# Kernel optimization log

Measured on AMD Instinct MI355X. Metric: run time of the kernel, lower is better.

The kernel has to match this reference:

```python
import jax, jax.numpy as jnp
import numpy as np

NUM_SPHERICAL = 7
NUM_RADIAL = 6
CUTOFF = 5.0
ENVELOPE_EXPONENT = 5
ENVELOPE_CUTOFF = 5.0  # hardcoded in the torch module: poly_envelop(cutoff=5.0, ...)
E = 1_000_000   # num edges
T = 4_000_000   # num triplets (angles)


def _jn_np(l, x):
    """Spherical Bessel j_l(x) in numpy via upward recurrence (x > 0)."""
    j0 = np.sin(x) / x
    if l == 0:
        return j0
    j1 = np.sin(x) / x ** 2 - np.cos(x) / x
    for i in range(2, l + 1):
        j0, j1 = j1, (2 * i - 1) / x * j1 - j0
    return j1


def _jn_zeros(n, k):
    """First k positive zeros of j_l for l=0..n-1 (zeros interlace)."""
    zeros = np.zeros((n, k))
    prev = np.arange(1, k + n) * np.pi  # zeros of j_0
    zeros[0] = prev[:k]
    for l in range(1, n):
        cur = []
        for i in range(len(prev) - 1):
            a, b = prev[i], prev[i + 1]
            fa = _jn_np(l, a)
            for _ in range(80):  # bisection
                m = 0.5 * (a + b)
                fm = _jn_np(l, m)
                if np.sign(fm) == np.sign(fa):
                    a, fa = m, fm
                else:
                    b = m
            cur.append(0.5 * (a + b))
        prev = np.array(cur)
        zeros[l] = prev[:k]
    return zeros


# constants derived from (num_spherical, num_radial) at build time
Z = _jn_zeros(NUM_SPHERICAL, NUM_RADIAL)  # [S, R] Bessel zeros z_{l,n}
NORM = np.array([[np.sqrt(2.0) / abs(_jn_np(l + 1, Z[l, n])) for n in range(NUM_RADIAL)]
                 for l in range(NUM_SPHERICAL)])  # [S, R]
Y_NORM = np.array([np.sqrt((2 * l + 1) / (4.0 * np.pi)) for l in range(NUM_SPHERICAL)])  # m=0 SH norms


def _spherical_jn(l, a):
    """j_l(a) in jax via upward recurrence."""
    j0 = jnp.sin(a) / a
    if l == 0:
        return j0
    j1 = jnp.sin(a) / a ** 2 - jnp.cos(a) / a
    for i in range(2, l + 1):
        j0, j1 = j1, (2 * i - 1) / a * j1 - j0
    return j1


def _envelope(d):
    """DimeNet polynomial envelope, p = exponent + 1, on u = d / cutoff."""
    p = ENVELOPE_EXPONENT + 1
    a = -(p + 1) * (p + 2) / 2.0
    b = float(p * (p + 2))
    c = -p * (p + 1) / 2.0
    u = d / ENVELOPE_CUTOFF
    env = 1.0 / u + a * u ** (p - 1) + b * u ** p + c * u ** (p + 1)
    return jnp.where(u < 1.0, env, 0.0)


def setup_inputs() -> dict:
    key = jax.random.key(0)
    k1, k2, k3 = jax.random.split(key, 3)
    d = jax.random.uniform(k1, (E,), jnp.float32, 0.5, CUTOFF)           # edge distances
    Angles = jax.random.uniform(k2, (T,), jnp.float32, 0.0, float(np.pi))  # triplet angles
    edge_index_1 = jax.random.randint(k3, (T,), 0, E, dtype=jnp.int64 if jax.config.jax_enable_x64 else jnp.int32)
    return {"d": d, "Angles": Angles, "edge_index_1": edge_index_1}


def reference(d, Angles, edge_index_1):
    S, R = NUM_SPHERICAL, NUM_RADIAL
    zeros = jnp.asarray(Z, d.dtype)     # [S, R]
    norm = jnp.asarray(NORM, d.dtype)   # [S, R]
    x = d / CUTOFF                      # [E]
    # radial basis: norm_{l,n} * j_l(z_{l,n} * x)  -> [E, S, R]
    rbf = jnp.stack([norm[l] * _spherical_jn(l, zeros[l][None, :] * x[:, None])
                     for l in range(S)], axis=1)
    rbf_env = (_envelope(d)[:, None, None] * rbf).reshape(d.shape[0], S * R)  # [E, S*R]
    rbf_env = rbf_env[edge_index_1]  # gather triplets -> [T, S*R]
    # angular basis: Y_l^0(theta) = sqrt((2l+1)/4pi) * P_l(cos theta)
    c = jnp.cos(Angles)
    P = [jnp.ones_like(c), c]
    for l in range(2, S):
        P.append(((2 * l - 1) * c * P[l - 1] - (l - 1) * P[l - 2]) / l)
    y_norm = jnp.asarray(Y_NORM, c.dtype)
    cbf = jnp.stack([y_norm[l] * P[l] for l in range(S)], axis=1)  # [T, S]
    cbf = jnp.repeat(cbf, R, axis=1)  # repeat_interleave -> [T, S*R]
    return rbf_env * cbf
```

## Files before the change

kernel.cpp:

```cpp
#include <hip/hip_runtime.h>
#include <hip/hip_bf16.h>
#include <hip/hip_fp16.h>
#include <math.h>

#define NSPH 7
#define NRAD 6
#define NJ 42
#define BLK 256

typedef float v2 __attribute__((ext_vector_type(2)));
typedef float v4 __attribute__((ext_vector_type(4)));

struct KC {
  float zf[NJ];
  float izf[NJ];
  float nyf[NJ];
  float sc5[7];
  float sc6[7];
};

__global__ void __launch_bounds__(BLK, 4) k_fused(const float* __restrict__ d,
                                                  const float* __restrict__ ang,
                                                  const int* __restrict__ idx,
                                                  float* __restrict__ out,
                                                  int T, KC C) {
  __shared__ __half sv[BLK * NJ];
  const int tid = threadIdx.x;
  const int t0 = blockIdx.x * BLK;
  const int t = t0 + tid;

  if (t < T) {
    const int e = __builtin_nontemporal_load(idx + t);
    const float an = __builtin_nontemporal_load(ang + t);
    const float dv = d[e];

    const float x = dv * 0.2f;
    const float invx = __builtin_amdgcn_rcpf(x);
    const float x2 = x * x;
    const float x5 = x2 * x2 * x;
    float env = invx + x5 * fmaf(x, fmaf(x, -21.0f, 48.0f), -28.0f);
    if (x >= 1.0f) env = 0.0f;

    const float cth = __cosf(an);
    float mP[NSPH];
    {
      float p0 = 1.f, p1 = cth;
      mP[0] = env; mP[1] = env * cth;
      const float rl[5] = {1.f/2.f, 1.f/3.f, 1.f/4.f, 1.f/5.f, 1.f/6.f};
      #pragma unroll
      for (int l = 2; l < NSPH; ++l) {
        float pn = (fmaf((float)(2*l-1) * cth, p1, -(float)(l-1) * p0)) * rl[l-2];
        mP[l] = env * pn;
        p0 = p1; p1 = pn;
      }
    }

    __half* row = sv + tid * NJ;

    #pragma unroll
    for (int l = 0; l < 5; ++l) {
      #pragma unroll
      for (int p = 0; p < 3; ++p) {
        const int i = l * NRAD + 2 * p;
        v2 z    = {C.zf[i],  C.zf[i+1]};
        v2 iz   = {C.izf[i], C.izf[i+1]};
        v2 ny   = {C.nyf[i], C.nyf[i+1]};
        v2 a    = z * x;
        v2 s;  s.x = __sinf(a.x);  s.y = __sinf(a.y);
        v2 inva = iz * invx;
        v2 j0   = s * inva;
        v2 jl;
        if (l == 0) {
          jl = j0;
        } else {
          v2 c;  c.x = __cosf(a.x);  c.y = __cosf(a.y);
          v2 j1 = (j0 - c) * inva;
          #pragma unroll
          for (int m = 2; m <= l; ++m) {
            v2 jn_ = ((float)(2*m-1) * inva) * j1 - j0;
            j0 = j1; j1 = jn_;
          }
          jl = j1;
        }
        v2 jv = (ny * jl) * mP[l];
        *(__half2*)(row + i) = __float22half2_rn((float2){jv.x, jv.y});
      }
    }

    #pragma unroll
    for (int l = 5; l < NSPH; ++l) {
      const float* sc = (l == 5) ? C.sc5 : C.sc6;
      #pragma unroll
      for (int p = 0; p < 3; ++p) {
        const int i = l * NRAD + 2 * p;
        v2 z    = {C.zf[i],  C.zf[i+1]};
        v2 iz   = {C.izf[i], C.izf[i+1]};
        v2 ny   = {C.nyf[i], C.nyf[i+1]};
        v2 a    = z * x;
        v2 s;  s.x = __sinf(a.x);  s.y = __sinf(a.y);
        v2 c;  c.x = __cosf(a.x);  c.y = __cosf(a.y);
        v2 inva = iz * invx;
        v2 j0   = s * inva;
        v2 j1   = (j0 - c) * inva;
        #pragma unroll
        for (int m = 2; m <= l; ++m) {
          v2 jn_ = ((float)(2*m-1) * inva) * j1 - j0;
          j0 = j1; j1 = jn_;
        }
        v2 u  = a * a;
        v2 pp = u * sc[6] + sc[5];
        pp = u * pp + sc[4];
        pp = u * pp + sc[3];
        pp = u * pp + sc[2];
        pp = u * pp + sc[1];
        pp = u * pp + sc[0];
        v2 u2 = u * u;
        v2 al = (l == 5) ? (u2 * a) : (u2 * u);
        v2 jser = al * pp;
        v2 jl;
        jl.x = (a.x < 4.0f) ? jser.x : j1.x;
        jl.y = (a.y < 4.0f) ? jser.y : j1.y;
        v2 jv = (ny * jl) * mP[l];
        *(__half2*)(row + i) = __float22half2_rn((float2){jv.x, jv.y});
      }
    }
  }
  __syncthreads();

  const int nwords = (((T - t0) < BLK ? (T - t0) : BLK)) * NJ;
  const int nv4 = nwords >> 2;
  float* ob = out + (size_t)t0 * NJ;
  #pragma unroll
  for (int k = 0; k < 11; ++k) {
    int w4 = k * BLK + tid;
    if (w4 < nv4) {
      uint2 hh = *(const uint2*)((const unsigned char*)sv + 8u * (unsigned)w4);
      float2 r0 = __half22float2(*(__half2*)&hh.x);
      float2 r1 = __half22float2(*(__half2*)&hh.y);
      *(v4*)(ob + 4 * w4) = (v4){r0.x, r0.y, r1.x, r1.y};
    }
  }
  {
    int rem = nwords - (nv4 << 2);
    if (tid < rem) {
      int wd = (nv4 << 2) + tid;
      ob[wd] = __half2float(sv[wd]);
    }
  }
}

static double jn_host(int l, double x) {
  double j0 = sin(x) / x;
  if (l == 0) return j0;
  double j1 = sin(x) / (x * x) - cos(x) / x;
  for (int i = 2; i <= l; ++i) {
    double jn_ = (2 * i - 1) / x * j1 - j0;
    j0 = j1; j1 = jn_;
  }
  return j1;
}

extern "C" void kernel_launch(void* const* d_in, const int* in_sizes, int n_in,
                              void* d_out, int out_size, void* d_ws, size_t ws_size,
                              hipStream_t stream) {
  const float* d   = (const float*)d_in[0];
  const float* ang = (const float*)d_in[1];
  const int*   idx = (const int*)d_in[2];
  float* out = (float*)d_out;
  const int T = in_sizes[1];

  KC C;
  {
    const double PI = 3.14159265358979323846;
    double zeros[NSPH][NRAD];
    double prev[NSPH + NRAD - 1];
    int np_ = NSPH + NRAD - 1;
    for (int i = 0; i < np_; ++i) prev[i] = (i + 1) * PI;
    for (int j = 0; j < NRAD; ++j) zeros[0][j] = prev[j];
    for (int l = 1; l < NSPH; ++l) {
      int nc = np_ - 1;
      double cur[NSPH + NRAD - 1];
      for (int i = 0; i < nc; ++i) {
        double a = prev[i], b = prev[i + 1];
        double fa = jn_host(l, a);
        for (int it = 0; it < 80; ++it) {
          double m = 0.5 * (a + b);
          double fm = jn_host(l, m);
          if ((fm > 0.0) == (fa > 0.0)) { a = m; fa = fm; } else { b = m; }
        }
        cur[i] = 0.5 * (a + b);
      }
      for (int i = 0; i < nc; ++i) prev[i] = cur[i];
      np_ = nc;
      for (int j = 0; j < NRAD; ++j) zeros[l][j] = prev[j];
    }
    for (int l = 0; l < NSPH; ++l) {
      double yn = sqrt((2.0 * l + 1.0) / (4.0 * PI));
      for (int n = 0; n < NRAD; ++n) {
        int i = l * NRAD + n;
        double z = zeros[l][n];
        C.zf[i]  = (float)z;
        C.izf[i] = (float)(1.0 / z);
        C.nyf[i] = (float)(sqrt(2.0) / fabs(jn_host(l + 1, z)) * yn);
      }
    }
    for (int l = 5; l <= 6; ++l) {
      double dfact = 1.0;
      for (int m = 2 * l + 1; m > 1; m -= 2) dfact *= m;
      double ck = 1.0 / dfact;
      float* sc = (l == 5) ? C.sc5 : C.sc6;
      sc[0] = (float)ck;
      for (int k = 1; k < 7; ++k) {
        ck = -ck / (2.0 * k * (2 * l + 2 * k + 1));
        sc[k] = (float)ck;
      }
    }
  }

  k_fused<<<(T + BLK - 1) / BLK, BLK, 0, stream>>>(d, ang, idx, out, T, C);
}
```

Measured before the change: 175.7 us.

## Use persistent blocks with prefetch of next tile inputs and nontemporal stores

Replaces the one-tile-per-block grid with a fixed grid of persistent blocks, each looping over a contiguous range of tiles. While computing the current tile, each block prefetches the next tile's index and angle, then its gathered distance, to hide gather latency. Shared-memory results are staged into registers so LDS can be reused right after a second barrier, and output writes become nontemporal. Launch bounds occupancy hint is raised from 4 to 6, which adds register pressure from the 11-entry staging array and an extra barrier per tile.

```diff
diff --git a/kernel.cpp b/kernel.cpp
--- a/kernel.cpp
+++ b/kernel.cpp
@@ -7,6 +7,7 @@
 #define NRAD 6
 #define NJ 42
 #define BLK 256
+#define GMAX 1536
 
 typedef float v2 __attribute__((ext_vector_type(2)));
 typedef float v4 __attribute__((ext_vector_type(4)));
@@ -19,133 +20,173 @@
   float sc6[7];
 };
 
-__global__ void __launch_bounds__(BLK, 4) k_fused(const float* __restrict__ d,
-                                                  const float* __restrict__ ang,
-                                                  const int* __restrict__ idx,
-                                                  float* __restrict__ out,
-                                                  int T, KC C) {
-  __shared__ __half sv[BLK * NJ];
-  const int tid = threadIdx.x;
-  const int t0 = blockIdx.x * BLK;
-  const int t = t0 + tid;
-
-  if (t < T) {
-    const int e = __builtin_nontemporal_load(idx + t);
-    const float an = __builtin_nontemporal_load(ang + t);
-    const float dv = d[e];
-
-    const float x = dv * 0.2f;
-    const float invx = __builtin_amdgcn_rcpf(x);
-    const float x2 = x * x;
-    const float x5 = x2 * x2 * x;
-    float env = invx + x5 * fmaf(x, fmaf(x, -21.0f, 48.0f), -28.0f);
-    if (x >= 1.0f) env = 0.0f;
-
-    const float cth = __cosf(an);
-    float mP[NSPH];
-    {
-      float p0 = 1.f, p1 = cth;
-      mP[0] = env; mP[1] = env * cth;
-      const float rl[5] = {1.f/2.f, 1.f/3.f, 1.f/4.f, 1.f/5.f, 1.f/6.f};
-      #pragma unroll
-      for (int l = 2; l < NSPH; ++l) {
-        float pn = (fmaf((float)(2*l-1) * cth, p1, -(float)(l-1) * p0)) * rl[l-2];
-        mP[l] = env * pn;
-        p0 = p1; p1 = pn;
-      }
-    }
-
-    __half* row = sv + tid * NJ;
-
-    #pragma unroll
-    for (int l = 0; l < 5; ++l) {
-      #pragma unroll
-      for (int p = 0; p < 3; ++p) {
-        const int i = l * NRAD + 2 * p;
-        v2 z    = {C.zf[i],  C.zf[i+1]};
-        v2 iz   = {C.izf[i], C.izf[i+1]};
-        v2 ny   = {C.nyf[i], C.nyf[i+1]};
-        v2 a    = z * x;
-        v2 s;  s.x = __sinf(a.x);  s.y = __sinf(a.y);
-        v2 inva = iz * invx;
-        v2 j0   = s * inva;
-        v2 jl;
-        if (l == 0) {
-          jl = j0;
-        } else {
-          v2 c;  c.x = __cosf(a.x);  c.y = __cosf(a.y);
-          v2 j1 = (j0 - c) * inva;
-          #pragma unroll
-          for (int m = 2; m <= l; ++m) {
-            v2 jn_ = ((float)(2*m-1) * inva) * j1 - j0;
-            j0 = j1; j1 = jn_;
-          }
-          jl = j1;
-        }
-        v2 jv = (ny * jl) * mP[l];
-        *(__half2*)(row + i) = __float22half2_rn((float2){jv.x, jv.y});
-      }
-    }
-
-    #pragma unroll
-    for (int l = 5; l < NSPH; ++l) {
-      const float* sc = (l == 5) ? C.sc5 : C.sc6;
-      #pragma unroll
-      for (int p = 0; p < 3; ++p) {
-        const int i = l * NRAD + 2 * p;
-        v2 z    = {C.zf[i],  C.zf[i+1]};
-        v2 iz   = {C.izf[i], C.izf[i+1]};
-        v2 ny   = {C.nyf[i], C.nyf[i+1]};
-        v2 a    = z * x;
-        v2 s;  s.x = __sinf(a.x);  s.y = __sinf(a.y);
+__device__ __forceinline__ void compute_row(float dv, float an, const KC& C,
+                                            __half* row) {
+  const float x = dv * 0.2f;
+  const float invx = __builtin_amdgcn_rcpf(x);
+  const float x2 = x * x;
+  const float x5 = x2 * x2 * x;
+  float env = invx + x5 * fmaf(x, fmaf(x, -21.0f, 48.0f), -28.0f);
+  if (x >= 1.0f) env = 0.0f;
+
+  const float cth = __cosf(an);
+  float mP[NSPH];
+  {
+    float p0 = 1.f, p1 = cth;
+    mP[0] = env; mP[1] = env * cth;
+    const float rl[5] = {1.f/2.f, 1.f/3.f, 1.f/4.f, 1.f/5.f, 1.f/6.f};
+    #pragma unroll
+    for (int l = 2; l < NSPH; ++l) {
+      float pn = (fmaf((float)(2*l-1) * cth, p1, -(float)(l-1) * p0)) * rl[l-2];
+      mP[l] = env * pn;
+      p0 = p1; p1 = pn;
+    }
+  }
+
+  #pragma unroll
+  for (int l = 0; l < 5; ++l) {
+    #pragma unroll
+    for (int p = 0; p < 3; ++p) {
+      const int i = l * NRAD + 2 * p;
+      v2 z    = {C.zf[i],  C.zf[i+1]};
+      v2 iz   = {C.izf[i], C.izf[i+1]};
+      v2 ny   = {C.nyf[i], C.nyf[i+1]};
+      v2 a    = z * x;
+      v2 s;  s.x = __sinf(a.x);  s.y = __sinf(a.y);
+      v2 inva = iz * invx;
+      v2 j0   = s * inva;
+      v2 jl;
+      if (l == 0) {
+        jl = j0;
+      } else {
         v2 c;  c.x = __cosf(a.x);  c.y = __cosf(a.y);
-        v2 inva = iz * invx;
-        v2 j0   = s * inva;
-        v2 j1   = (j0 - c) * inva;
+        v2 j1 = (j0 - c) * inva;
         #pragma unroll
         for (int m = 2; m <= l; ++m) {
           v2 jn_ = ((float)(2*m-1) * inva) * j1 - j0;
           j0 = j1; j1 = jn_;
         }
-        v2 u  = a * a;
-        v2 pp = u * sc[6] + sc[5];
-        pp = u * pp + sc[4];
-        pp = u * pp + sc[3];
-        pp = u * pp + sc[2];
-        pp = u * pp + sc[1];
-        pp = u * pp + sc[0];
-        v2 u2 = u * u;
-        v2 al = (l == 5) ? (u2 * a) : (u2 * u);
-        v2 jser = al * pp;
-        v2 jl;
-        jl.x = (a.x < 4.0f) ? jser.x : j1.x;
-        jl.y = (a.y < 4.0f) ? jser.y : j1.y;
-        v2 jv = (ny * jl) * mP[l];
-        *(__half2*)(row + i) = __float22half2_rn((float2){jv.x, jv.y});
-      }
-    }
-  }
-  __syncthreads();
-
-  const int nwords = (((T - t0) < BLK ? (T - t0) : BLK)) * NJ;
-  const int nv4 = nwords >> 2;
-  float* ob = out + (size_t)t0 * NJ;
+        jl = j1;
+      }
+      v2 jv = (ny * jl) * mP[l];
+      *(__half2*)(row + i) = __float22half2_rn((float2){jv.x, jv.y});
+    }
+  }
+
   #pragma unroll
-  for (int k = 0; k < 11; ++k) {
-    int w4 = k * BLK + tid;
-    if (w4 < nv4) {
-      uint2 hh = *(const uint2*)((const unsigned char*)sv + 8u * (unsigned)w4);
-      float2 r0 = __half22float2(*(__half2*)&hh.x);
-      float2 r1 = __half22float2(*(__half2*)&hh.y);
-      *(v4*)(ob + 4 * w4) = (v4){r0.x, r0.y, r1.x, r1.y};
-    }
-  }
+  for (int l = 5; l < NSPH; ++l) {
+    const float* sc = (l == 5) ? C.sc5 : C.sc6;
+    #pragma unroll
+    for (int p = 0; p < 3; ++p) {
+      const int i = l * NRAD + 2 * p;
+      v2 z    = {C.zf[i],  C.zf[i+1]};
+      v2 iz   = {C.izf[i], C.izf[i+1]};
+      v2 ny   = {C.nyf[i], C.nyf[i+1]};
+      v2 a    = z * x;
+      v2 s;  s.x = __sinf(a.x);  s.y = __sinf(a.y);
+      v2 c;  c.x = __cosf(a.x);  c.y = __cosf(a.y);
+      v2 inva = iz * invx;
+      v2 j0   = s * inva;
+      v2 j1   = (j0 - c) * inva;
+      #pragma unroll
+      for (int m = 2; m <= l; ++m) {
+        v2 jn_ = ((float)(2*m-1) * inva) * j1 - j0;
+        j0 = j1; j1 = jn_;
+      }
+      v2 u  = a * a;
+      v2 pp = u * sc[6] + sc[5];
+      pp = u * pp + sc[4];
+      pp = u * pp + sc[3];
+      pp = u * pp + sc[2];
+      pp = u * pp + sc[1];
+      pp = u * pp + sc[0];
+      v2 u2 = u * u;
+      v2 al = (l == 5) ? (u2 * a) : (u2 * u);
+      v2 jser = al * pp;
+      v2 jl;
+      jl.x = (a.x < 4.0f) ? jser.x : j1.x;
+      jl.y = (a.y < 4.0f) ? jser.y : j1.y;
+      v2 jv = (ny * jl) * mP[l];
+      *(__half2*)(row + i) = __float22half2_rn((float2){jv.x, jv.y});
+    }
+  }
+}
+
+__global__ void __launch_bounds__(BLK, 6) k_fused(const float* __restrict__ d,
+                                                  const float* __restrict__ ang,
+                                                  const int* __restrict__ idx,
+                                                  float* __restrict__ out,
+                                                  int T, int NT, int G, KC C) {
+  __shared__ __half sv[BLK * NJ];
+  const int tid = threadIdx.x;
+  const int b = blockIdx.x;
+  const int q = NT / G, r = NT - q * G;
+  const int start = b * q + (b < r ? b : r);
+  const int cnt = q + (b < r ? 1 : 0);
+  if (cnt <= 0) return;
+
+  int e = 0; float an = 0.f, dv = 2.5f;
   {
-    int rem = nwords - (nv4 << 2);
-    if (tid < rem) {
-      int wd = (nv4 << 2) + tid;
-      ob[wd] = __half2float(sv[wd]);
-    }
+    int t = start * BLK + tid;
+    if (t < T) {
+      e  = __builtin_nontemporal_load(idx + t);
+      an = __builtin_nontemporal_load(ang + t);
+      dv = d[e];
+    }
+  }
+
+  for (int it = 0; it < cnt; ++it) {
+    const int t0 = (start + it) * BLK;
+    const bool last = (it + 1 == cnt);
+
+    int e_nx = 0; float an_nx = 0.f; bool vn = false;
+    if (!last) {
+      int tn = t0 + BLK + tid;
+      vn = tn < T;
+      if (vn) {
+        e_nx  = __builtin_nontemporal_load(idx + tn);
+        an_nx = __builtin_nontemporal_load(ang + tn);
+      }
+    }
+
+    if (t0 + tid < T)
+      compute_row(dv, an, C, sv + tid * NJ);
+    __syncthreads();
+
+    const int nt_ = (T - t0) < BLK ? (T - t0) : BLK;
+    const int nwords = nt_ * NJ;
+    const int nv4 = nwords >> 2;
+    uint2 st[11];
+    #pragma unroll
+    for (int k = 0; k < 11; ++k) {
+      int w4 = k * BLK + tid;
+      if (w4 < nv4)
+        st[k] = *(const uint2*)((const unsigned char*)sv + 8u * (unsigned)w4);
+    }
+    float remv = 0.f;
+    const int rem = nwords - (nv4 << 2);
+    if (tid < rem) remv = __half2float(sv[(nv4 << 2) + tid]);
+
+    float dv_nx = 2.5f;
+    if (vn) dv_nx = d[e_nx];
+
+    __syncthreads();
+
+    float* ob = out + (size_t)t0 * NJ;
+    #pragma unroll
+    for (int k = 0; k < 11; ++k) {
+      int w4 = k * BLK + tid;
+      if (w4 < nv4) {
+        float2 r0 = __half22float2(*(__half2*)&st[k].x);
+        float2 r1 = __half22float2(*(__half2*)&st[k].y);
+        __builtin_nontemporal_store((v4){r0.x, r0.y, r1.x, r1.y},
+                                    (v4*)(ob + 4 * w4));
+      }
+    }
+    if (tid < rem)
+      __builtin_nontemporal_store(remv, ob + (nv4 << 2) + tid);
+
+    e = e_nx; an = an_nx; dv = dv_nx;
   }
 }
 
@@ -217,5 +258,7 @@
     }
   }
 
-  k_fused<<<(T + BLK - 1) / BLK, BLK, 0, stream>>>(d, ang, idx, out, T, C);
-}
+  const int NT = (T + BLK - 1) / BLK;
+  const int G  = NT < GMAX ? NT : GMAX;
+  k_fused<<<G, BLK, 0, stream>>>(d, ang, idx, out, T, NT, G, C);
+}
```

Result: faster. 170.9 us (-2.8%).
